# Performance work log

Measured on AMD Instinct MI355X. Metric: run time of the kernel, lower is better.

## Reference

```python
import jax, jax.numpy as jnp
import numpy as np

N_NODES = 100000
N_EDGES = 1250000
CH = [64, 64, 64]


def setup_inputs() -> dict:
    key = jax.random.key(0)
    ks = jax.random.split(key, 12)
    inp = {
        "x": jax.random.normal(ks[0], (N_NODES, CH[0]), dtype=jnp.float32),
        "edge_index": jax.random.randint(ks[1], (2, N_EDGES), 0, N_NODES, dtype=jnp.int64),
    }
    # Per-layer SAGEConv params (PyG default: out = lin_l(mean_aggr) + lin_r(x), bias only on lin_l)
    # plus per-channel PReLU weight (torch default init 0.25).
    for i in range(2):
        cin, cout = CH[i], CH[i + 1]
        s = 1.0 / np.sqrt(cin)
        inp[f"w_l{i}"] = jax.random.uniform(ks[2 + 4 * i], (cin, cout), jnp.float32, -s, s)
        inp[f"b_l{i}"] = jax.random.uniform(ks[3 + 4 * i], (cout,), jnp.float32, -s, s)
        inp[f"w_r{i}"] = jax.random.uniform(ks[4 + 4 * i], (cin, cout), jnp.float32, -s, s)
        inp[f"a{i}"] = jnp.full((cout,), 0.25, dtype=jnp.float32)
    return inp


def _sage_prelu(x, src, dst, w_l, b_l, w_r, a):
    n = x.shape[0]
    # mean aggregation of source features at destination nodes
    agg = jax.ops.segment_sum(x[src], dst, num_segments=n)  # [N, Cin]
    cnt = jax.ops.segment_sum(jnp.ones_like(dst, dtype=x.dtype), dst, num_segments=n)
    agg = agg / jnp.maximum(cnt, 1.0)[:, None]
    h = agg @ w_l + b_l + x @ w_r  # [N, Cout]
    return jnp.where(h >= 0, h, a * h)  # channel-wise PReLU


def reference(x, edge_index, w_l0, b_l0, w_r0, a0, w_l1, b_l1, w_r1, a1):
    src, dst = edge_index[0], edge_index[1]
    h = _sage_prelu(x, src, dst, w_l0, b_l0, w_r0, a0)
    h = _sage_prelu(h, src, dst, w_l1, b_l1, w_r1, a1)
    return h
```

## Files before the change

### kernel.cpp

```cpp
#include <hip/hip_runtime.h>
#include <hip/hip_fp16.h>

#define N_NODES 100000
#define N_EDGES 1250000
#define C 64
#define NPB 128
#define NB 782
#define CAP 2048
#define P1_CHUNKQ 2048
#define P1_BLOCKS 153

typedef int vint4 __attribute__((ext_vector_type(4)));

__global__ __launch_bounds__(256) void partition_kernel(
        const int* __restrict__ src, const int* __restrict__ dst,
        int* __restrict__ gcnt, unsigned int* __restrict__ packed) {
    __shared__ int hist[NB];
    __shared__ int gbase[NB];
    const int t = threadIdx.x;
    for (int i = t; i < NB; i += 256) hist[i] = 0;
    __syncthreads();

    const int qbase = blockIdx.x * P1_CHUNKQ;
    const int NQ = N_EDGES / 4;
    const vint4* d4 = (const vint4*)dst;
    const vint4* s4 = (const vint4*)src;

    for (int i = 0; i < P1_CHUNKQ; i += 256) {
        int q = qbase + i + t;
        if (q < NQ) {
            vint4 d = __builtin_nontemporal_load(&d4[q]);
            atomicAdd(&hist[d.x >> 7], 1);
            atomicAdd(&hist[d.y >> 7], 1);
            atomicAdd(&hist[d.z >> 7], 1);
            atomicAdd(&hist[d.w >> 7], 1);
        }
    }
    __syncthreads();

    for (int b = t; b < NB; b += 256) {
        int h = hist[b];
        gbase[b] = (h > 0) ? (b * CAP + atomicAdd(&gcnt[b], h)) : 0;
        hist[b] = 0;
    }
    __syncthreads();

    for (int i = 0; i < P1_CHUNKQ; i += 256) {
        int q = qbase + i + t;
        if (q < NQ) {
            vint4 d = __builtin_nontemporal_load(&d4[q]);
            vint4 s = __builtin_nontemporal_load(&s4[q]);
            int bb, lp, pos;
            bb = d.x >> 7; lp = atomicAdd(&hist[bb], 1); pos = gbase[bb] + lp;
            if (pos < (bb + 1) * CAP) packed[pos] = ((unsigned)s.x << 7) | (unsigned)(d.x & 127);
            bb = d.y >> 7; lp = atomicAdd(&hist[bb], 1); pos = gbase[bb] + lp;
            if (pos < (bb + 1) * CAP) packed[pos] = ((unsigned)s.y << 7) | (unsigned)(d.y & 127);
            bb = d.z >> 7; lp = atomicAdd(&hist[bb], 1); pos = gbase[bb] + lp;
            if (pos < (bb + 1) * CAP) packed[pos] = ((unsigned)s.z << 7) | (unsigned)(d.z & 127);
            bb = d.w >> 7; lp = atomicAdd(&hist[bb], 1); pos = gbase[bb] + lp;
            if (pos < (bb + 1) * CAP) packed[pos] = ((unsigned)s.w << 7) | (unsigned)(d.w & 127);
        }
    }
}

__global__ __launch_bounds__(1024) void scan_gcnt_kernel(const int* __restrict__ gcnt,
                                                         int* __restrict__ bbase,
                                                         int* __restrict__ offsets) {
    __shared__ int s[1024];
    int t = threadIdx.x;
    int v = (t < NB) ? gcnt[t] : 0;
    s[t] = v;
    __syncthreads();
    for (int off = 1; off < 1024; off <<= 1) {
        int u = (t >= off) ? s[t - off] : 0;
        __syncthreads();
        s[t] += u;
        __syncthreads();
    }
    if (t < NB) bbase[t] = s[t] - v;
    if (t == 0) offsets[N_NODES] = N_EDGES;
}

__global__ __launch_bounds__(256) void sort_kernel(
        const unsigned int* __restrict__ packed,
        const int* __restrict__ gcnt, const int* __restrict__ bbase,
        int* __restrict__ offsets, int* __restrict__ sorted_src) {
    __shared__ unsigned int s_e[CAP];
    __shared__ int s_hist[NPB];
    __shared__ int s_excl[NPB];
    const int b = blockIdx.x;
    const int t = threadIdx.x;
    const int nb = min(gcnt[b], CAP);
    const int base = bbase[b];

    for (int i = t; i < NPB; i += 256) s_hist[i] = 0;
    __syncthreads();
    for (int i = t; i < nb; i += 256) {
        unsigned int u = packed[(size_t)b * CAP + i];
        s_e[i] = u;
        atomicAdd(&s_hist[u & 127u], 1);
    }
    __syncthreads();
    if (t < NPB) s_excl[t] = s_hist[t];
    __syncthreads();
    for (int off = 1; off < NPB; off <<= 1) {
        int v = (t < NPB && t >= off) ? s_excl[t - off] : 0;
        __syncthreads();
        if (t < NPB) s_excl[t] += v;
        __syncthreads();
    }
    if (t < NPB) {
        int excl = s_excl[t] - s_hist[t];
        s_hist[t] = excl;
        int node = b * NPB + t;
        if (node < N_NODES) offsets[node] = base + excl;
    }
    __syncthreads();
    for (int i = t; i < nb; i += 256) {
        unsigned int u = s_e[i];
        int lp = atomicAdd(&s_hist[u & 127u], 1);
        sorted_src[base + lp] = (int)(u >> 7);
    }
}

__global__ __launch_bounds__(256) void dense_kernel(
        const float* x,
        const float* __restrict__ wl, const float* __restrict__ wr,
        const float* __restrict__ bl,
        __half* __restrict__ z, float* r, int n_nodes) {
    __shared__ float s_w[C][2 * C];
    __shared__ float s_x[64][C + 1];

    const int t = threadIdx.x;
    const int base = blockIdx.x * 64;

    for (int i = t; i < C * C; i += 256) {
        int k = i >> 6, c = i & 63;
        s_w[k][c] = wl[i];
        s_w[k][64 + c] = wr[i];
    }
    for (int i = t; i < 1024; i += 256) {
        int n = i >> 4;
        int kq = i & 15;
        float4 v = make_float4(0.f, 0.f, 0.f, 0.f);
        if (base + n < n_nodes) v = ((const float4*)x)[((size_t)(base + n) << 4) + kq];
        s_x[n][kq * 4 + 0] = v.x;
        s_x[n][kq * 4 + 1] = v.y;
        s_x[n][kq * 4 + 2] = v.z;
        s_x[n][kq * 4 + 3] = v.w;
    }
    __syncthreads();

    const int lane = t & 63;
    const int wv = t >> 6;
    const int cg = lane & 15;
    const int q = lane >> 4;
    const int n0 = wv * 16 + 4 * q;

    float4 bv = ((const float4*)bl)[cg];
    float accz[4][4];
    float accr[4][4];
#pragma unroll
    for (int i = 0; i < 4; ++i) {
        accz[i][0] = accz[i][1] = accz[i][2] = accz[i][3] = 0.f;
        accr[i][0] = bv.x; accr[i][1] = bv.y; accr[i][2] = bv.z; accr[i][3] = bv.w;
    }

#pragma unroll 8
    for (int k = 0; k < C; ++k) {
        float4 wlv = *(const float4*)&s_w[k][4 * cg];
        float4 wrv = *(const float4*)&s_w[k][64 + 4 * cg];
        float xk[4];
#pragma unroll
        for (int i = 0; i < 4; ++i) xk[i] = s_x[n0 + i][k];
#pragma unroll
        for (int i = 0; i < 4; ++i) {
            accz[i][0] += xk[i] * wlv.x;
            accz[i][1] += xk[i] * wlv.y;
            accz[i][2] += xk[i] * wlv.z;
            accz[i][3] += xk[i] * wlv.w;
            accr[i][0] += xk[i] * wrv.x;
            accr[i][1] += xk[i] * wrv.y;
            accr[i][2] += xk[i] * wrv.z;
            accr[i][3] += xk[i] * wrv.w;
        }
    }

#pragma unroll
    for (int i = 0; i < 4; ++i) {
        size_t gn = (size_t)base + n0 + i;
        if (gn < (size_t)n_nodes) {
            __half2 p0 = __float22half2_rn(make_float2(accz[i][0], accz[i][1]));
            __half2 p1 = __float22half2_rn(make_float2(accz[i][2], accz[i][3]));
            ((__half2*)z)[gn * 32 + 2 * cg + 0] = p0;
            ((__half2*)z)[gn * 32 + 2 * cg + 1] = p1;
            ((float4*)r)[gn * 16 + cg] = make_float4(accr[i][0], accr[i][1], accr[i][2], accr[i][3]);
        }
    }
}

__global__ __launch_bounds__(256) void gather_kernel(
        const __half* __restrict__ z,
        const float* r,
        const int* __restrict__ offsets,
        const int* __restrict__ sorted_src,
        const float* __restrict__ a,
        float* out) {
    const int lane = threadIdx.x & 63;
    const int node = (blockIdx.x << 2) + (threadIdx.x >> 6);

    const int beg = offsets[node];
    const int deg = offsets[node + 1] - beg;

    float acc = 0.0f;
    for (int j = 0; j < deg; j += 8) {
        int last = deg - 1;
        int s0 = sorted_src[beg + min(j + 0, last)];
        int s1 = sorted_src[beg + min(j + 1, last)];
        int s2 = sorted_src[beg + min(j + 2, last)];
        int s3 = sorted_src[beg + min(j + 3, last)];
        int s4 = sorted_src[beg + min(j + 4, last)];
        int s5 = sorted_src[beg + min(j + 5, last)];
        int s6 = sorted_src[beg + min(j + 6, last)];
        int s7 = sorted_src[beg + min(j + 7, last)];
        float v0 = __half2float(z[(size_t)s0 * C + lane]);
        float v1 = __half2float(z[(size_t)s1 * C + lane]);
        float v2 = __half2float(z[(size_t)s2 * C + lane]);
        float v3 = __half2float(z[(size_t)s3 * C + lane]);
        float v4 = __half2float(z[(size_t)s4 * C + lane]);
        float v5 = __half2float(z[(size_t)s5 * C + lane]);
        float v6 = __half2float(z[(size_t)s6 * C + lane]);
        float v7 = __half2float(z[(size_t)s7 * C + lane]);
        float sum = v0;
        sum += (j + 1 < deg) ? v1 : 0.0f;
        sum += (j + 2 < deg) ? v2 : 0.0f;
        sum += (j + 3 < deg) ? v3 : 0.0f;
        sum += (j + 4 < deg) ? v4 : 0.0f;
        sum += (j + 5 < deg) ? v5 : 0.0f;
        sum += (j + 6 < deg) ? v6 : 0.0f;
        sum += (j + 7 < deg) ? v7 : 0.0f;
        acc += sum;
    }
    float rv = r[(size_t)node * C + lane];
    float h = acc / (float)max(deg, 1) + rv;
    float av = a[lane];
    out[(size_t)node * C + lane] = h >= 0.0f ? h : av * h;
}

extern "C" void kernel_launch(void* const* d_in, const int* in_sizes, int n_in,
                              void* d_out, int out_size, void* d_ws, size_t ws_size,
                              hipStream_t stream) {
    const float* x    = (const float*)d_in[0];
    const int*   ei   = (const int*)d_in[1];
    const float* w_l0 = (const float*)d_in[2];
    const float* b_l0 = (const float*)d_in[3];
    const float* w_r0 = (const float*)d_in[4];
    const float* a0   = (const float*)d_in[5];
    const float* w_l1 = (const float*)d_in[6];
    const float* b_l1 = (const float*)d_in[7];
    const float* w_r1 = (const float*)d_in[8];
    const float* a1   = (const float*)d_in[9];
    float* out = (float*)d_out;

    const int* src = ei;
    const int* dst = ei + N_EDGES;

    int* gcnt            = (int*)d_ws;
    int* bbase           = gcnt + 1024;
    int* offsets         = bbase + 1024;
    unsigned int* packed = (unsigned int*)(offsets + (N_NODES + 1));
    int* sorted_src      = (int*)(packed + (size_t)NB * CAP);
    __half* Z            = (__half*)(sorted_src + N_EDGES);
    float* B             = (float*)(Z + (size_t)N_NODES * C);

    hipMemsetAsync(gcnt, 0, 1024 * sizeof(int), stream);

    const int dblocks = (N_NODES + 63) / 64;
    const int nblocks = N_NODES / 4;

    partition_kernel<<<P1_BLOCKS, 256, 0, stream>>>(src, dst, gcnt, packed);
    scan_gcnt_kernel<<<1, 1024, 0, stream>>>(gcnt, bbase, offsets);
    sort_kernel<<<NB, 256, 0, stream>>>(packed, gcnt, bbase, offsets, sorted_src);

    dense_kernel<<<dblocks, 256, 0, stream>>>(x, w_l0, w_r0, b_l0, Z, B, N_NODES);
    gather_kernel<<<nblocks, 256, 0, stream>>>(Z, B, offsets, sorted_src, a0, B);

    dense_kernel<<<dblocks, 256, 0, stream>>>(B, w_l1, w_r1, b_l1, Z, B, N_NODES);
    gather_kernel<<<nblocks, 256, 0, stream>>>(Z, B, offsets, sorted_src, a1, out);
}
```

Before: 279.6 us.

## Store intermediates in fp16, fuse bucket scan into sort, register-cache partition edges

Several changes land together. The partition kernel keeps loaded edges in registers so they are read once, and uses per-wave shared histograms. The separate scan kernel is removed, with each sort block computing its own base by reducing the earlier bucket counts. The root term and the layer-1 activations are stored as fp16 instead of fp32 to cut memory traffic, and the gather loop drops its clamped tail handling for a remainder loop. The fp16 storage adds rounding error, and each sort block now does a redundant prefix read over up to 782 counts.

```diff
diff --git a/kernel.cpp b/kernel.cpp
--- a/kernel.cpp
+++ b/kernel.cpp
@@ -9,89 +9,90 @@
 #define CAP 2048
 #define P1_CHUNKQ 2048
 #define P1_BLOCKS 153
+#define NQ (N_EDGES / 4)
 
 typedef int vint4 __attribute__((ext_vector_type(4)));
 
 __global__ __launch_bounds__(256) void partition_kernel(
         const int* __restrict__ src, const int* __restrict__ dst,
         int* __restrict__ gcnt, unsigned int* __restrict__ packed) {
-    __shared__ int hist[NB];
-    __shared__ int gbase[NB];
+    __shared__ int s_hist[4][NB];
+    __shared__ int s_cur[NB];
     const int t = threadIdx.x;
-    for (int i = t; i < NB; i += 256) hist[i] = 0;
+    const int w = t >> 6;
+    for (int i = t; i < 4 * NB; i += 256) ((int*)s_hist)[i] = 0;
     __syncthreads();
 
     const int qbase = blockIdx.x * P1_CHUNKQ;
-    const int NQ = N_EDGES / 4;
     const vint4* d4 = (const vint4*)dst;
     const vint4* s4 = (const vint4*)src;
 
-    for (int i = 0; i < P1_CHUNKQ; i += 256) {
-        int q = qbase + i + t;
-        if (q < NQ) {
-            vint4 d = __builtin_nontemporal_load(&d4[q]);
-            atomicAdd(&hist[d.x >> 7], 1);
-            atomicAdd(&hist[d.y >> 7], 1);
-            atomicAdd(&hist[d.z >> 7], 1);
-            atomicAdd(&hist[d.w >> 7], 1);
+    vint4 dreg[8], sreg[8];
+    bool val[8];
+#pragma unroll
+    for (int k = 0; k < 8; ++k) {
+        int q = qbase + k * 256 + t;
+        val[k] = q < NQ;
+        if (val[k]) {
+            dreg[k] = __builtin_nontemporal_load(&d4[q]);
+            sreg[k] = __builtin_nontemporal_load(&s4[q]);
+        }
+    }
+
+#pragma unroll
+    for (int k = 0; k < 8; ++k) {
+        if (val[k]) {
+            atomicAdd(&s_hist[w][dreg[k].x >> 7], 1);
+            atomicAdd(&s_hist[w][dreg[k].y >> 7], 1);
+            atomicAdd(&s_hist[w][dreg[k].z >> 7], 1);
+            atomicAdd(&s_hist[w][dreg[k].w >> 7], 1);
         }
     }
     __syncthreads();
 
     for (int b = t; b < NB; b += 256) {
-        int h = hist[b];
-        gbase[b] = (h > 0) ? (b * CAP + atomicAdd(&gcnt[b], h)) : 0;
-        hist[b] = 0;
-    }
-    __syncthreads();
-
-    for (int i = 0; i < P1_CHUNKQ; i += 256) {
-        int q = qbase + i + t;
-        if (q < NQ) {
-            vint4 d = __builtin_nontemporal_load(&d4[q]);
-            vint4 s = __builtin_nontemporal_load(&s4[q]);
-            int bb, lp, pos;
-            bb = d.x >> 7; lp = atomicAdd(&hist[bb], 1); pos = gbase[bb] + lp;
-            if (pos < (bb + 1) * CAP) packed[pos] = ((unsigned)s.x << 7) | (unsigned)(d.x & 127);
-            bb = d.y >> 7; lp = atomicAdd(&hist[bb], 1); pos = gbase[bb] + lp;
-            if (pos < (bb + 1) * CAP) packed[pos] = ((unsigned)s.y << 7) | (unsigned)(d.y & 127);
-            bb = d.z >> 7; lp = atomicAdd(&hist[bb], 1); pos = gbase[bb] + lp;
-            if (pos < (bb + 1) * CAP) packed[pos] = ((unsigned)s.z << 7) | (unsigned)(d.z & 127);
-            bb = d.w >> 7; lp = atomicAdd(&hist[bb], 1); pos = gbase[bb] + lp;
-            if (pos < (bb + 1) * CAP) packed[pos] = ((unsigned)s.w << 7) | (unsigned)(d.w & 127);
-        }
-    }
-}
-
-__global__ __launch_bounds__(1024) void scan_gcnt_kernel(const int* __restrict__ gcnt,
-                                                         int* __restrict__ bbase,
-                                                         int* __restrict__ offsets) {
-    __shared__ int s[1024];
-    int t = threadIdx.x;
-    int v = (t < NB) ? gcnt[t] : 0;
-    s[t] = v;
-    __syncthreads();
-    for (int off = 1; off < 1024; off <<= 1) {
-        int u = (t >= off) ? s[t - off] : 0;
-        __syncthreads();
-        s[t] += u;
-        __syncthreads();
-    }
-    if (t < NB) bbase[t] = s[t] - v;
-    if (t == 0) offsets[N_NODES] = N_EDGES;
+        int tot = s_hist[0][b] + s_hist[1][b] + s_hist[2][b] + s_hist[3][b];
+        s_cur[b] = (tot > 0) ? (b * CAP + atomicAdd(&gcnt[b], tot)) : 0;
+    }
+    __syncthreads();
+
+#pragma unroll
+    for (int k = 0; k < 8; ++k) {
+        if (val[k]) {
+            int bb, pos;
+            bb = dreg[k].x >> 7; pos = atomicAdd(&s_cur[bb], 1);
+            if (pos < (bb + 1) * CAP) packed[pos] = ((unsigned)sreg[k].x << 7) | (unsigned)(dreg[k].x & 127);
+            bb = dreg[k].y >> 7; pos = atomicAdd(&s_cur[bb], 1);
+            if (pos < (bb + 1) * CAP) packed[pos] = ((unsigned)sreg[k].y << 7) | (unsigned)(dreg[k].y & 127);
+            bb = dreg[k].z >> 7; pos = atomicAdd(&s_cur[bb], 1);
+            if (pos < (bb + 1) * CAP) packed[pos] = ((unsigned)sreg[k].z << 7) | (unsigned)(dreg[k].z & 127);
+            bb = dreg[k].w >> 7; pos = atomicAdd(&s_cur[bb], 1);
+            if (pos < (bb + 1) * CAP) packed[pos] = ((unsigned)sreg[k].w << 7) | (unsigned)(dreg[k].w & 127);
+        }
+    }
 }
 
 __global__ __launch_bounds__(256) void sort_kernel(
         const unsigned int* __restrict__ packed,
-        const int* __restrict__ gcnt, const int* __restrict__ bbase,
+        const int* __restrict__ gcnt,
         int* __restrict__ offsets, int* __restrict__ sorted_src) {
+    __shared__ int s_part[256];
     __shared__ unsigned int s_e[CAP];
     __shared__ int s_hist[NPB];
     __shared__ int s_excl[NPB];
     const int b = blockIdx.x;
     const int t = threadIdx.x;
+
+    int psum = 0;
+    for (int i = t; i < b; i += 256) psum += gcnt[i];
+    s_part[t] = psum;
+    __syncthreads();
+    for (int off = 128; off > 0; off >>= 1) {
+        if (t < off) s_part[t] += s_part[t + off];
+        __syncthreads();
+    }
+    const int base = s_part[0];
     const int nb = min(gcnt[b], CAP);
-    const int base = bbase[b];
 
     for (int i = t; i < NPB; i += 256) s_hist[i] = 0;
     __syncthreads();
@@ -121,13 +122,15 @@
         int lp = atomicAdd(&s_hist[u & 127u], 1);
         sorted_src[base + lp] = (int)(u >> 7);
     }
-}
-
+    if (b == NB - 1 && t == 0) offsets[N_NODES] = N_EDGES;
+}
+
+template <typename XT>
 __global__ __launch_bounds__(256) void dense_kernel(
-        const float* x,
+        const XT* __restrict__ x,
         const float* __restrict__ wl, const float* __restrict__ wr,
         const float* __restrict__ bl,
-        __half* __restrict__ z, float* r, int n_nodes) {
+        __half* __restrict__ z, __half* __restrict__ r, int n_nodes) {
     __shared__ float s_w[C][2 * C];
     __shared__ float s_x[64][C + 1];
 
@@ -139,15 +142,27 @@
         s_w[k][c] = wl[i];
         s_w[k][64 + c] = wr[i];
     }
-    for (int i = t; i < 1024; i += 256) {
-        int n = i >> 4;
-        int kq = i & 15;
-        float4 v = make_float4(0.f, 0.f, 0.f, 0.f);
-        if (base + n < n_nodes) v = ((const float4*)x)[((size_t)(base + n) << 4) + kq];
-        s_x[n][kq * 4 + 0] = v.x;
-        s_x[n][kq * 4 + 1] = v.y;
-        s_x[n][kq * 4 + 2] = v.z;
-        s_x[n][kq * 4 + 3] = v.w;
+    if constexpr (sizeof(XT) == 4) {
+        for (int i = t; i < 1024; i += 256) {
+            int n = i >> 4;
+            int kq = i & 15;
+            float4 v = make_float4(0.f, 0.f, 0.f, 0.f);
+            if (base + n < n_nodes) v = ((const float4*)x)[((size_t)(base + n) << 4) + kq];
+            s_x[n][kq * 4 + 0] = v.x;
+            s_x[n][kq * 4 + 1] = v.y;
+            s_x[n][kq * 4 + 2] = v.z;
+            s_x[n][kq * 4 + 3] = v.w;
+        }
+    } else {
+        for (int i = t; i < 2048; i += 256) {
+            int n = i >> 5;
+            int c2 = i & 31;
+            float2 f = make_float2(0.f, 0.f);
+            if (base + n < n_nodes)
+                f = __half22float2(((const __half2*)x)[(size_t)(base + n) * 32 + c2]);
+            s_x[n][2 * c2 + 0] = f.x;
+            s_x[n][2 * c2 + 1] = f.y;
+        }
     }
     __syncthreads();
 
@@ -190,39 +205,40 @@
     for (int i = 0; i < 4; ++i) {
         size_t gn = (size_t)base + n0 + i;
         if (gn < (size_t)n_nodes) {
-            __half2 p0 = __float22half2_rn(make_float2(accz[i][0], accz[i][1]));
-            __half2 p1 = __float22half2_rn(make_float2(accz[i][2], accz[i][3]));
-            ((__half2*)z)[gn * 32 + 2 * cg + 0] = p0;
-            ((__half2*)z)[gn * 32 + 2 * cg + 1] = p1;
-            ((float4*)r)[gn * 16 + cg] = make_float4(accr[i][0], accr[i][1], accr[i][2], accr[i][3]);
-        }
-    }
-}
-
+            ((__half2*)z)[gn * 32 + 2 * cg + 0] = __float22half2_rn(make_float2(accz[i][0], accz[i][1]));
+            ((__half2*)z)[gn * 32 + 2 * cg + 1] = __float22half2_rn(make_float2(accz[i][2], accz[i][3]));
+            ((__half2*)r)[gn * 32 + 2 * cg + 0] = __float22half2_rn(make_float2(accr[i][0], accr[i][1]));
+            ((__half2*)r)[gn * 32 + 2 * cg + 1] = __float22half2_rn(make_float2(accr[i][2], accr[i][3]));
+        }
+    }
+}
+
+template <typename OT>
 __global__ __launch_bounds__(256) void gather_kernel(
         const __half* __restrict__ z,
-        const float* r,
+        const __half* __restrict__ r,
         const int* __restrict__ offsets,
         const int* __restrict__ sorted_src,
         const float* __restrict__ a,
-        float* out) {
+        OT* __restrict__ out) {
     const int lane = threadIdx.x & 63;
     const int node = (blockIdx.x << 2) + (threadIdx.x >> 6);
 
     const int beg = offsets[node];
     const int deg = offsets[node + 1] - beg;
+    const int deg8 = deg & ~7;
 
     float acc = 0.0f;
-    for (int j = 0; j < deg; j += 8) {
-        int last = deg - 1;
-        int s0 = sorted_src[beg + min(j + 0, last)];
-        int s1 = sorted_src[beg + min(j + 1, last)];
-        int s2 = sorted_src[beg + min(j + 2, last)];
-        int s3 = sorted_src[beg + min(j + 3, last)];
-        int s4 = sorted_src[beg + min(j + 4, last)];
-        int s5 = sorted_src[beg + min(j + 5, last)];
-        int s6 = sorted_src[beg + min(j + 6, last)];
-        int s7 = sorted_src[beg + min(j + 7, last)];
+    int j = 0;
+    for (; j < deg8; j += 8) {
+        int s0 = sorted_src[beg + j + 0];
+        int s1 = sorted_src[beg + j + 1];
+        int s2 = sorted_src[beg + j + 2];
+        int s3 = sorted_src[beg + j + 3];
+        int s4 = sorted_src[beg + j + 4];
+        int s5 = sorted_src[beg + j + 5];
+        int s6 = sorted_src[beg + j + 6];
+        int s7 = sorted_src[beg + j + 7];
         float v0 = __half2float(z[(size_t)s0 * C + lane]);
         float v1 = __half2float(z[(size_t)s1 * C + lane]);
         float v2 = __half2float(z[(size_t)s2 * C + lane]);
@@ -231,20 +247,19 @@
         float v5 = __half2float(z[(size_t)s5 * C + lane]);
         float v6 = __half2float(z[(size_t)s6 * C + lane]);
         float v7 = __half2float(z[(size_t)s7 * C + lane]);
-        float sum = v0;
-        sum += (j + 1 < deg) ? v1 : 0.0f;
-        sum += (j + 2 < deg) ? v2 : 0.0f;
-        sum += (j + 3 < deg) ? v3 : 0.0f;
-        sum += (j + 4 < deg) ? v4 : 0.0f;
-        sum += (j + 5 < deg) ? v5 : 0.0f;
-        sum += (j + 6 < deg) ? v6 : 0.0f;
-        sum += (j + 7 < deg) ? v7 : 0.0f;
-        acc += sum;
-    }
-    float rv = r[(size_t)node * C + lane];
+        acc += ((v0 + v1) + (v2 + v3)) + ((v4 + v5) + (v6 + v7));
+    }
+    for (; j < deg; ++j)
+        acc += __half2float(z[(size_t)sorted_src[beg + j] * C + lane]);
+
+    float rv = __half2float(r[(size_t)node * C + lane]);
     float h = acc / (float)max(deg, 1) + rv;
     float av = a[lane];
-    out[(size_t)node * C + lane] = h >= 0.0f ? h : av * h;
+    float o = h >= 0.0f ? h : av * h;
+    if constexpr (sizeof(OT) == 2)
+        out[(size_t)node * C + lane] = __float2half(o);
+    else
+        out[(size_t)node * C + lane] = o;
 }
 
 extern "C" void kernel_launch(void* const* d_in, const int* in_sizes, int n_in,
@@ -266,12 +281,12 @@
     const int* dst = ei + N_EDGES;
 
     int* gcnt            = (int*)d_ws;
-    int* bbase           = gcnt + 1024;
-    int* offsets         = bbase + 1024;
+    int* offsets         = gcnt + 1024;
     unsigned int* packed = (unsigned int*)(offsets + (N_NODES + 1));
     int* sorted_src      = (int*)(packed + (size_t)NB * CAP);
     __half* Z            = (__half*)(sorted_src + N_EDGES);
-    float* B             = (float*)(Z + (size_t)N_NODES * C);
+    __half* R            = Z + (size_t)N_NODES * C;
+    __half* H            = R + (size_t)N_NODES * C;
 
     hipMemsetAsync(gcnt, 0, 1024 * sizeof(int), stream);
 
@@ -279,12 +294,11 @@
     const int nblocks = N_NODES / 4;
 
     partition_kernel<<<P1_BLOCKS, 256, 0, stream>>>(src, dst, gcnt, packed);
-    scan_gcnt_kernel<<<1, 1024, 0, stream>>>(gcnt, bbase, offsets);
-    sort_kernel<<<NB, 256, 0, stream>>>(packed, gcnt, bbase, offsets, sorted_src);
-
-    dense_kernel<<<dblocks, 256, 0, stream>>>(x, w_l0, w_r0, b_l0, Z, B, N_NODES);
-    gather_kernel<<<nblocks, 256, 0, stream>>>(Z, B, offsets, sorted_src, a0, B);
-
-    dense_kernel<<<dblocks, 256, 0, stream>>>(B, w_l1, w_r1, b_l1, Z, B, N_NODES);
-    gather_kernel<<<nblocks, 256, 0, stream>>>(Z, B, offsets, sorted_src, a1, out);
-}
+    sort_kernel<<<NB, 256, 0, stream>>>(packed, gcnt, offsets, sorted_src);
+
+    dense_kernel<float><<<dblocks, 256, 0, stream>>>(x, w_l0, w_r0, b_l0, Z, R, N_NODES);
+    gather_kernel<__half><<<nblocks, 256, 0, stream>>>(Z, R, offsets, sorted_src, a0, H);
+
+    dense_kernel<__half><<<dblocks, 256, 0, stream>>>(H, w_l1, w_r1, b_l1, Z, R, N_NODES);
+    gather_kernel<float><<<nblocks, 256, 0, stream>>>(Z, R, offsets, sorted_src, a1, out);
+}
```

Measured after the change: 298.7 us. 6.9% more time.
